# Performance work log

Hardware: AMD Instinct MI355X
Metric: run time of the kernel (lower is better)

## Reference

```python
import jax, jax.numpy as jnp
import numpy as np


def setup_inputs() -> dict:
    key = jax.random.key(0)
    k1, k2, k3, k4 = jax.random.split(key, 4)
    B, L, C, F = 64, 4096, 256, 128
    t = jax.random.uniform(k1, (B, L), dtype=jnp.float32)
    freqs = jax.random.normal(k2, (F,), dtype=jnp.float32)
    amp_sin = jax.random.normal(k3, (C, F), dtype=jnp.float32)
    amp_cos = jax.random.normal(k4, (C, F), dtype=jnp.float32)
    return {"t": t, "freqs": freqs, "amp_sin": amp_sin, "amp_cos": amp_cos}


def reference(t, freqs, amp_sin, amp_cos):
    # angles: (B, L, F) = 2*pi * freqs * t  (broadcast over last dim)
    angles = (2.0 * jnp.pi) * t[..., None] * freqs  # (B, L, F)
    # sum over frequencies with per-channel amplitudes is a GEMM:
    # out[b,l,c] = sum_f sin(angles)[b,l,f]*amp_sin[c,f] + cos(angles)[b,l,f]*amp_cos[c,f]
    out = jnp.einsum('blf,cf->blc', jnp.sin(angles), amp_sin)
    out = out + jnp.einsum('blf,cf->blc', jnp.cos(angles), amp_cos)
    return out  # (B, L, C)
```

## Files before the change

### kernel.cpp

```cpp
#include <hip/hip_runtime.h>
#include <stdint.h>


typedef __bf16 bf16x8 __attribute__((ext_vector_type(8)));
typedef float  floatx4 __attribute__((ext_vector_type(4)));

#define MT    64
#define F_    128
#define C_    256
#define LSTR  264
#define TPB   8

#define LDS_BARRIER() asm volatile("s_waitcnt lgkmcnt(0)\n\ts_barrier" ::: "memory")

__global__ __launch_bounds__(256, 2)
void fourier_fused(const float* __restrict__ t,
                   const float* __restrict__ freqs,
                   const float* __restrict__ amp_sin,
                   const float* __restrict__ amp_cos,
                   float* __restrict__ out)
{
    __shared__ __align__(16) __bf16 Af[2][MT * LSTR];

    const int tid  = threadIdx.x;
    const int wave = tid >> 6;
    const int lane = tid & 63;
    const int l15  = lane & 15;
    const int quad = lane >> 4;
    const int n0   = wave * 64;

    const int fgrp = tid & 15;
    const int rsub = tid >> 4;

    const int tile0 = blockIdx.x * TPB;

    float tv[4];
    #pragma unroll
    for (int p = 0; p < 4; ++p)
        tv[p] = t[tile0 * MT + p * 16 + rsub];

    const float4 f0v = *(const float4*)(freqs + fgrp * 8);
    const float4 f1v = *(const float4*)(freqs + fgrp * 8 + 4);
    const float fr[8] = {f0v.x, f0v.y, f0v.z, f0v.w, f1v.x, f1v.y, f1v.z, f1v.w};

    bf16x8 b[8][4];
    #pragma unroll
    for (int ks = 0; ks < 8; ++ks) {
        const float* __restrict__ amp = (ks < 4) ? amp_sin : amp_cos;
        const int f0 = (ks & 3) * 32 + quad * 8;
        #pragma unroll
        for (int ni = 0; ni < 4; ++ni) {
            const float* p = amp + (n0 + ni * 16 + l15) * F_ + f0;
            const float4 b0 = *(const float4*)(p);
            const float4 b1 = *(const float4*)(p + 4);
            b[ks][ni][0] = (__bf16)b0.x; b[ks][ni][1] = (__bf16)b0.y;
            b[ks][ni][2] = (__bf16)b0.z; b[ks][ni][3] = (__bf16)b0.w;
            b[ks][ni][4] = (__bf16)b1.x; b[ks][ni][5] = (__bf16)b1.y;
            b[ks][ni][6] = (__bf16)b1.z; b[ks][ni][7] = (__bf16)b1.w;
        }
    }

    #pragma unroll 2
    for (int it = 0; it < TPB; ++it) {
        const int m0 = (tile0 + it) * MT;
        __bf16* __restrict__ A = Af[it & 1];

        float tvn[4];
        {
            const int mb = (it + 1 < TPB) ? (m0 + MT) : tile0 * MT;
            #pragma unroll
            for (int p = 0; p < 4; ++p)
                tvn[p] = t[mb + p * 16 + rsub];
        }

        #pragma unroll
        for (int pass = 0; pass < 4; ++pass) {
            const int ml = pass * 16 + rsub;
            const float tval = tv[pass];
            bf16x8 sv, cv;
            #pragma unroll
            for (int j = 0; j < 8; ++j) {
                const float r = __builtin_amdgcn_fractf(tval * fr[j]);
                sv[j] = (__bf16)__builtin_amdgcn_sinf(r);
                cv[j] = (__bf16)__builtin_amdgcn_cosf(r);
            }
            *(bf16x8*)&A[ml * LSTR + fgrp * 8]      = sv;
            *(bf16x8*)&A[ml * LSTR + F_ + fgrp * 8] = cv;
        }
        LDS_BARRIER();

        #pragma unroll
        for (int mi = 0; mi < 4; ++mi) {
            floatx4 acc[4];
            #pragma unroll
            for (int ni = 0; ni < 4; ++ni)
                acc[ni] = (floatx4){0.f, 0.f, 0.f, 0.f};

            #pragma unroll
            for (int ks = 0; ks < 8; ++ks) {
                const bf16x8 a =
                    *(const bf16x8*)&A[(mi * 16 + l15) * LSTR + ks * 32 + quad * 8];
                #pragma unroll
                for (int ni = 0; ni < 4; ++ni)
                    acc[ni] = __builtin_amdgcn_mfma_f32_16x16x32_bf16(
                        b[ks][ni], a, acc[ni], 0, 0, 0);
            }

            #pragma unroll
            for (int ni = 0; ni < 4; ++ni) {
                float* p = out + (size_t)(m0 + mi * 16 + l15) * C_
                               + n0 + ni * 16 + quad * 4;
                *(floatx4*)p = acc[ni];
            }
        }

        #pragma unroll
        for (int p = 0; p < 4; ++p) tv[p] = tvn[p];
    }
}

extern "C" void kernel_launch(void* const* d_in, const int* in_sizes, int n_in,
                              void* d_out, int out_size, void* d_ws, size_t ws_size,
                              hipStream_t stream) {
    const float* t   = (const float*)d_in[0];
    const float* fq  = (const float*)d_in[1];
    const float* As  = (const float*)d_in[2];
    const float* Ac  = (const float*)d_in[3];
    float* outp      = (float*)d_out;

    const int M = in_sizes[0];
    hipLaunchKernelGGL(fourier_fused, dim3(M / (MT * TPB)), dim3(256), 0, stream,
                       t, fq, As, Ac, outp);
}
```

Measured before the change: 281.3 us.

## Software-pipeline sin/cos generation of next tile with MFMA on current tile

Adds a prologue that computes the first tile's sin/cos into LDS, then in each iteration computes the next tile's sin/cos into the alternate LDS buffer, interleaved per 16-row slice with the MFMA work on the current buffer. This lets transcendental VALU work overlap with matrix-core work and leaves one barrier per iteration, placed after the compute. The A fragments for each slice are preloaded into registers, which raises register pressure and could hurt occupancy at 2 waves per SIMD.

```diff
diff --git a/kernel.cpp b/kernel.cpp
--- a/kernel.cpp
+++ b/kernel.cpp
@@ -34,11 +34,6 @@
 
     const int tile0 = blockIdx.x * TPB;
 
-    float tv[4];
-    #pragma unroll
-    for (int p = 0; p < 4; ++p)
-        tv[p] = t[tile0 * MT + p * 16 + rsub];
-
     const float4 f0v = *(const float4*)(freqs + fgrp * 8);
     const float4 f1v = *(const float4*)(freqs + fgrp * 8 + 4);
     const float fr[8] = {f0v.x, f0v.y, f0v.z, f0v.w, f1v.x, f1v.y, f1v.z, f1v.w};
@@ -60,51 +55,77 @@
         }
     }
 
+    float tprod[4];
+    #pragma unroll
+    for (int p = 0; p < 4; ++p)
+        tprod[p] = t[tile0 * MT + p * 16 + rsub];
+
+    #pragma unroll
+    for (int pass = 0; pass < 4; ++pass) {
+        const float tval = tprod[pass];
+        bf16x8 sv, cv;
+        #pragma unroll
+        for (int j = 0; j < 8; ++j) {
+            const float r = __builtin_amdgcn_fractf(tval * fr[j]);
+            sv[j] = (__bf16)__builtin_amdgcn_sinf(r);
+            cv[j] = (__bf16)__builtin_amdgcn_cosf(r);
+        }
+        *(bf16x8*)&Af[0][(pass * 16 + rsub) * LSTR + fgrp * 8]      = sv;
+        *(bf16x8*)&Af[0][(pass * 16 + rsub) * LSTR + F_ + fgrp * 8] = cv;
+    }
+
+    #pragma unroll
+    for (int p = 0; p < 4; ++p)
+        tprod[p] = t[(tile0 + 1) * MT + p * 16 + rsub];
+
+    LDS_BARRIER();
+
     #pragma unroll 2
     for (int it = 0; it < TPB; ++it) {
-        const int m0 = (tile0 + it) * MT;
-        __bf16* __restrict__ A = Af[it & 1];
+        const int m0   = (tile0 + it) * MT;
+        const int cur  = it & 1;
+        const int nxt  = cur ^ 1;
+        const bool prod = (it + 1 < TPB);
 
-        float tvn[4];
+        float tnext[4];
         {
-            const int mb = (it + 1 < TPB) ? (m0 + MT) : tile0 * MT;
+            const int mb = (it + 2 < TPB) ? (m0 + 2 * MT) : tile0 * MT;
             #pragma unroll
             for (int p = 0; p < 4; ++p)
-                tvn[p] = t[mb + p * 16 + rsub];
+                tnext[p] = t[mb + p * 16 + rsub];
         }
 
         #pragma unroll
-        for (int pass = 0; pass < 4; ++pass) {
-            const int ml = pass * 16 + rsub;
-            const float tval = tv[pass];
-            bf16x8 sv, cv;
+        for (int mi = 0; mi < 4; ++mi) {
+            bf16x8 a[8];
             #pragma unroll
-            for (int j = 0; j < 8; ++j) {
-                const float r = __builtin_amdgcn_fractf(tval * fr[j]);
-                sv[j] = (__bf16)__builtin_amdgcn_sinf(r);
-                cv[j] = (__bf16)__builtin_amdgcn_cosf(r);
+            for (int ks = 0; ks < 8; ++ks)
+                a[ks] = *(const bf16x8*)
+                    &Af[cur][(mi * 16 + l15) * LSTR + ks * 32 + quad * 8];
+
+            if (prod) {
+                const float tval = tprod[mi];
+                bf16x8 sv, cv;
+                #pragma unroll
+                for (int j = 0; j < 8; ++j) {
+                    const float r = __builtin_amdgcn_fractf(tval * fr[j]);
+                    sv[j] = (__bf16)__builtin_amdgcn_sinf(r);
+                    cv[j] = (__bf16)__builtin_amdgcn_cosf(r);
+                }
+                *(bf16x8*)&Af[nxt][(mi * 16 + rsub) * LSTR + fgrp * 8]      = sv;
+                *(bf16x8*)&Af[nxt][(mi * 16 + rsub) * LSTR + F_ + fgrp * 8] = cv;
             }
-            *(bf16x8*)&A[ml * LSTR + fgrp * 8]      = sv;
-            *(bf16x8*)&A[ml * LSTR + F_ + fgrp * 8] = cv;
-        }
-        LDS_BARRIER();
 
-        #pragma unroll
-        for (int mi = 0; mi < 4; ++mi) {
             floatx4 acc[4];
             #pragma unroll
             for (int ni = 0; ni < 4; ++ni)
                 acc[ni] = (floatx4){0.f, 0.f, 0.f, 0.f};
-
             #pragma unroll
-            for (int ks = 0; ks < 8; ++ks) {
-                const bf16x8 a =
-                    *(const bf16x8*)&A[(mi * 16 + l15) * LSTR + ks * 32 + quad * 8];
+            for (int ks = 0; ks < 8; ++ks)
                 #pragma unroll
                 for (int ni = 0; ni < 4; ++ni)
                     acc[ni] = __builtin_amdgcn_mfma_f32_16x16x32_bf16(
-                        b[ks][ni], a, acc[ni], 0, 0, 0);
-            }
+                        b[ks][ni], a[ks], acc[ni], 0, 0, 0);
 
             #pragma unroll
             for (int ni = 0; ni < 4; ++ni) {
@@ -114,8 +135,10 @@
             }
         }
 
+        LDS_BARRIER();
+
         #pragma unroll
-        for (int p = 0; p < 4; ++p) tv[p] = tvn[p];
+        for (int p = 0; p < 4; ++p) tprod[p] = tnext[p];
     }
 }
 
```

New measurement: 279.2 us. About the same (-0.8%).
